# Kernel optimization log

Measured on AMD Instinct MI355X. Metric: run time of the kernel, lower is better.

The kernel has to match this reference:

```python
import jax, jax.numpy as jnp
import numpy as np
from jax import lax

P = 8  # DFFN patch_size


def _ln(x, w, b):
    # WithBias LayerNorm over channel dim of NCHW (matches to_3d -> LN(-1) -> to_4d)
    mu = x.mean(1, keepdims=True)
    var = ((x - mu) ** 2).mean(1, keepdims=True)
    return (x - mu) / jnp.sqrt(var + 1e-5) * w[None, :, None, None] + b[None, :, None, None]


def _conv1x1(x, w, b=None):
    y = jnp.einsum('bchw,oc->bohw', x, w)
    if b is not None:
        y = y + b[None, :, None, None]
    return y


def setup_inputs() -> dict:
    key = jax.random.key(0)
    ks = jax.random.split(key, 9)
    B, C, H, W = 2, 64, 96, 96
    hid = C  # ffn_expansion_factor = 1
    s = lambda k, shape, scale=0.05: jax.random.normal(k, shape, jnp.float32) * scale
    return {
        'x': s(ks[0], (B, C, H, W), 1.0),
        'ln1_w': jnp.ones((C,), jnp.float32), 'ln1_b': jnp.zeros((C,), jnp.float32),
        'ln2_w': jnp.ones((C,), jnp.float32), 'ln2_b': jnp.zeros((C,), jnp.float32),
        'q_w': s(ks[1], (C, C)), 'q_b': jnp.zeros((C,), jnp.float32),
        'k_w': s(ks[2], (C, C)), 'k_b': jnp.zeros((C,), jnp.float32),
        'v_w': s(ks[3], (C, C)), 'v_b': jnp.zeros((C,), jnp.float32),
        'fft_w': s(ks[4], (hid, P, P // 2 + 1), 1.0),
        'proj_in_w': s(ks[5], (hid, C)),
        'dw_w': s(ks[6], (hid, 1, 3, 3)),
        'proj_out_w': s(ks[7], (C, hid // 2)),
    }


def reference(x, ln1_w, ln1_b, ln2_w, ln2_b, q_w, q_b, k_w, k_b, v_w, v_b,
              fft_w, proj_in_w, dw_w, proj_out_w):
    B, C, H, W = x.shape
    # --- attention sub-block (unscaled spatial self-attn) ---
    xn = _ln(x, ln1_w, ln1_b)
    q = _conv1x1(xn, q_w, q_b).reshape(B, C, H * W)
    k = _conv1x1(xn, k_w, k_b).reshape(B, C, H * W)
    v = _conv1x1(xn, v_w, v_b).reshape(B, C, H * W)
    attn = jax.nn.softmax(jnp.einsum('bcn,bcm->bnm', q, k), axis=-1)  # [B, HW, HW]
    out = jnp.einsum('bcm,bnm->bcn', v, attn).reshape(B, C, H, W)
    x = x + out
    # --- DFFN sub-block ---
    xn = _ln(x, ln2_w, ln2_b)
    h = _conv1x1(xn, proj_in_w)  # hidden == C (expansion factor 1)
    hid = h.shape[1]
    hb, wb = H // P, W // P
    hp = h.reshape(B, hid, hb, P, wb, P).transpose(0, 2, 4, 1, 3, 5)  # [B,hb,wb,hid,P,P]
    hf = jnp.fft.rfft2(hp) * fft_w  # real learned spectral filter
    hp = jnp.fft.irfft2(hf, s=(P, P))
    h = hp.transpose(0, 3, 1, 4, 2, 5).reshape(B, hid, H, W)
    h = lax.conv_general_dilated(h, dw_w, (1, 1), ((1, 1), (1, 1)),
                                 feature_group_count=hid,
                                 dimension_numbers=('NCHW', 'OIHW', 'NCHW'))
    h1, h2 = jnp.split(h, 2, axis=1)
    h = jax.nn.gelu(h1, approximate=False) * h2  # torch F.gelu is exact erf
    return x + _conv1x1(h, proj_out_w)
```

## Files before the change

kernel.cpp:

```cpp
#include <hip/hip_runtime.h>
#include <hip/hip_bf16.h>
#include <math.h>

#define CH 64
#define NPOS 9216
#define NTOT 18432
#define NSPLIT 8
#define TILES_PER_SPLIT 18
#define LOG2E 1.4426950408889634f

typedef short bf16x8 __attribute__((ext_vector_type(8)));
typedef short bf16x4 __attribute__((ext_vector_type(4)));
typedef float f32x4 __attribute__((ext_vector_type(4)));
typedef int   i32x4 __attribute__((ext_vector_type(4)));
typedef int   i32x2 __attribute__((ext_vector_type(2)));
typedef unsigned int u32;

__device__ __forceinline__ float bf2f(short s) {
  unsigned int u = ((unsigned int)(unsigned short)s) << 16;
  return __builtin_bit_cast(float, u);
}
__device__ __forceinline__ short f2bf(float f) {
  unsigned int u = __builtin_bit_cast(unsigned int, f);
  unsigned int r = (u + 0x7fffu + ((u >> 16) & 1u)) >> 16;
  return (short)r;
}
__device__ __forceinline__ float gelu_exact(float x) {
  return 0.5f * x * (1.f + erff(x * 0.70710678118654752440f));
}


__global__ __launch_bounds__(256) void k_ln_qkv(
    const float* __restrict__ x, const float* __restrict__ ln1w, const float* __restrict__ ln1b,
    const float* __restrict__ qw, const float* __restrict__ qb,
    const float* __restrict__ kw, const float* __restrict__ kb,
    const float* __restrict__ vw, const float* __restrict__ vb,
    short* __restrict__ Qg, short* __restrict__ Kg, short* __restrict__ Vgt) {
  int mat = blockIdx.y;
  int half = blockIdx.z;
  const float* wsrc = (mat == 0) ? qw : (mat == 1) ? kw : vw;
  const float* bsrc = (mat == 0) ? qb : (mat == 1) ? kb : vb;
  int idx = blockIdx.x * 256 + threadIdx.x;
  int b = idx / NPOS, n = idx % NPOS;
  const float* xb = x + (size_t)b * CH * NPOS + n;
  float xr[64];
  float mu = 0.f;
#pragma unroll
  for (int c = 0; c < 64; ++c) { float v = xb[c * NPOS]; xr[c] = v; mu += v; }
  mu *= (1.f / 64.f);
  float var = 0.f;
#pragma unroll
  for (int c = 0; c < 64; ++c) { float d = xr[c] - mu; var += d * d; }
  float rstd = rsqrtf(var * (1.f / 64.f) + 1e-5f);
#pragma unroll
  for (int c = 0; c < 64; ++c) xr[c] = (xr[c] - mu) * rstd * ln1w[c] + ln1b[c];
  if (mat == 2) {
    for (int o2 = 0; o2 < 4; ++o2) {
#pragma unroll
      for (int j = 0; j < 8; ++j) {
        int o = half * 32 + o2 * 8 + j;
        float acc = bsrc[o];
        const float* wrow = wsrc + o * 64;
#pragma unroll
        for (int c = 0; c < 64; ++c) acc += wrow[c] * xr[c];
        Vgt[(size_t)o * NTOT + idx] = f2bf(acc);
      }
    }
  } else {
    float kscale = (mat == 1) ? LOG2E : 1.f;
    short* outp = ((mat == 0) ? Qg : Kg) + (size_t)idx * 64 + half * 32;
    for (int o2 = 0; o2 < 4; ++o2) {
      bf16x8 v8;
#pragma unroll
      for (int j = 0; j < 8; ++j) {
        int o = half * 32 + o2 * 8 + j;
        float acc = bsrc[o];
        const float* wrow = wsrc + o * 64;
#pragma unroll
        for (int c = 0; c < 64; ++c) acc += wrow[c] * xr[c];
        v8[j] = f2bf(acc * kscale);
      }
      *(bf16x8*)(outp + o2 * 8) = v8;
    }
  }
}

#define LDPK 80
#define LDP  72
__global__ __launch_bounds__(512) void k_attn(
    const short* __restrict__ Qg, const short* __restrict__ Kg, const short* __restrict__ Vgt,
    u32* __restrict__ PoT, float* __restrict__ Pl) {
  __shared__ __align__(16) short Kt[2][64 * LDPK];
  __shared__ __align__(16) short Vt[2][64 * LDP];
  int b = blockIdx.y;
  int n0 = blockIdx.x * 256;
  int ks = blockIdx.z;
  int tid = threadIdx.x;
  int w = tid >> 6, lane = tid & 63;
  int L = lane & 15, quad = lane >> 4;

  bf16x8 qa[2][2];
#pragma unroll
  for (int qt = 0; qt < 2; ++qt) {
    const short* qb_ = Qg + ((size_t)(b * NPOS + n0 + w * 32 + qt * 16 + L)) * 64;
    qa[qt][0] = *(const bf16x8*)(qb_ + quad * 8);
    qa[qt][1] = *(const bf16x8*)(qb_ + 32 + quad * 8);
  }

  f32x4 o[2][4];
#pragma unroll
  for (int qt = 0; qt < 2; ++qt)
#pragma unroll
    for (int nb = 0; nb < 4; ++nb) o[qt][nb] = (f32x4){0.f, 0.f, 0.f, 0.f};
  float rl[2] = {0.f, 0.f};

  int ck = tid & 7, rk = tid >> 3;
  int c8 = tid & 7, dr = tid >> 3;
  int vslot = (c8 >> 2) * 32 + (c8 & 1) * 16 + ((c8 >> 1) & 1) * 4;
  i32x4 kr, vr;
  {
    int kt = ks * TILES_PER_SPLIT;
    kr = ((const i32x4*)(Kg + ((size_t)(b * NPOS + kt * 64)) * 64))[tid];
    vr = *(const i32x4*)(Vgt + (size_t)b * NPOS + kt * 64 + c8 * 8 + (size_t)dr * NTOT);
    ((i32x4*)Kt[0])[rk * 10 + ck] = kr;
    short* vrow = Vt[0] + dr * LDP + vslot;
    *(i32x2*)(vrow) = (i32x2){vr[0], vr[1]};
    *(i32x2*)(vrow + 8) = (i32x2){vr[2], vr[3]};
  }

  for (int t = 0; t < TILES_PER_SPLIT; ++t) {
    int cur = t & 1;
    if (t + 1 < TILES_PER_SPLIT) {
      int kt = ks * TILES_PER_SPLIT + t + 1;
      kr = ((const i32x4*)(Kg + ((size_t)(b * NPOS + kt * 64)) * 64))[tid];
      vr = *(const i32x4*)(Vgt + (size_t)b * NPOS + kt * 64 + c8 * 8 + (size_t)dr * NTOT);
    }
    __syncthreads();

    const i32x4* kt4 = (const i32x4*)Kt[cur];
    const short* vt = Vt[cur];
    __builtin_amdgcn_s_setprio(1);
#pragma unroll
    for (int kp = 0; kp < 2; ++kp) {
      u32 pw0[4], pw1[4];
#pragma unroll
      for (int h = 0; h < 2; ++h) {
        int kti = kp * 2 + h;
        bf16x8 kf0 = __builtin_bit_cast(bf16x8, kt4[(kti * 16 + L) * 10 + quad]);
        bf16x8 kf1 = __builtin_bit_cast(bf16x8, kt4[(kti * 16 + L) * 10 + 4 + quad]);
#pragma unroll
        for (int qt = 0; qt < 2; ++qt) {
          f32x4 st = {0.f, 0.f, 0.f, 0.f};
          st = __builtin_amdgcn_mfma_f32_16x16x32_bf16(kf0, qa[qt][0], st, 0, 0, 0);
          st = __builtin_amdgcn_mfma_f32_16x16x32_bf16(kf1, qa[qt][1], st, 0, 0, 0);
          float p0 = __builtin_amdgcn_exp2f(st[0]);
          float p1 = __builtin_amdgcn_exp2f(st[1]);
          float p2 = __builtin_amdgcn_exp2f(st[2]);
          float p3 = __builtin_amdgcn_exp2f(st[3]);
          rl[qt] += (p0 + p1) + (p2 + p3);
          u32 lo = __builtin_amdgcn_perm(__builtin_bit_cast(u32, p1), __builtin_bit_cast(u32, p0), 0x07060302u);
          u32 hi = __builtin_amdgcn_perm(__builtin_bit_cast(u32, p3), __builtin_bit_cast(u32, p2), 0x07060302u);
          if (qt == 0) { pw0[h * 2] = lo; pw0[h * 2 + 1] = hi; }
          else         { pw1[h * 2] = lo; pw1[h * 2 + 1] = hi; }
        }
      }
      i32x4 pq0 = {(int)pw0[0], (int)pw0[1], (int)pw0[2], (int)pw0[3]};
      i32x4 pq1 = {(int)pw1[0], (int)pw1[1], (int)pw1[2], (int)pw1[3]};
      bf16x8 pp0 = __builtin_bit_cast(bf16x8, pq0);
      bf16x8 pp1 = __builtin_bit_cast(bf16x8, pq1);
#pragma unroll
      for (int nb = 0; nb < 4; ++nb) {
        bf16x8 va8 = *(const bf16x8*)(vt + (nb * 16 + L) * LDP + kp * 32 + quad * 8);
        o[0][nb] = __builtin_amdgcn_mfma_f32_16x16x32_bf16(va8, pp0, o[0][nb], 0, 0, 0);
        o[1][nb] = __builtin_amdgcn_mfma_f32_16x16x32_bf16(va8, pp1, o[1][nb], 0, 0, 0);
      }
    }
    __builtin_amdgcn_s_setprio(0);

    if (t + 1 < TILES_PER_SPLIT) {
      int nxt = 1 - cur;
      ((i32x4*)Kt[nxt])[rk * 10 + ck] = kr;
      short* vrow = Vt[nxt] + dr * LDP + vslot;
      *(i32x2*)(vrow) = (i32x2){vr[0], vr[1]};
      *(i32x2*)(vrow + 8) = (i32x2){vr[2], vr[3]};
    }
  }

#pragma unroll
  for (int qt = 0; qt < 2; ++qt) {
    rl[qt] += __shfl_xor(rl[qt], 16);
    rl[qt] += __shfl_xor(rl[qt], 32);
  }

#pragma unroll
  for (int qt = 0; qt < 2; ++qt) {
    int qg = b * NPOS + n0 + w * 32 + qt * 16 + L;
#pragma unroll
    for (int nb = 0; nb < 4; ++nb)
#pragma unroll
      for (int ip = 0; ip < 2; ++ip) {
        u32 pk = ((u32)(unsigned short)f2bf(o[qt][nb][2 * ip + 1]) << 16) |
                 (u32)(unsigned short)f2bf(o[qt][nb][2 * ip]);
        int d32 = nb * 8 + quad * 2 + ip;
        PoT[((size_t)(ks * 32 + d32)) * NTOT + qg] = pk;
      }
    if (quad == 0) Pl[(size_t)ks * NTOT + qg] = rl[qt];
  }
}

__global__ __launch_bounds__(256) void k_res_ln2_proj(
    const float* __restrict__ x, const u32* __restrict__ PoT, const float* __restrict__ Pl,
    const float* __restrict__ ln2w, const float* __restrict__ ln2b,
    const float* __restrict__ piw,
    float* __restrict__ X2, float* __restrict__ Hbuf) {
  __shared__ float s1a[4 * 64], s2a[4 * 64];
  __shared__ __align__(16) short xn[64 * 72];
  int t = threadIdx.x;
  int w = t >> 6;
  int p = t & 63;
  int q0 = blockIdx.x * 64;
  int q = q0 + p;
  int b = q / NPOS;
  int nn = q0 % NPOS;
  int n = q % NPOS;

  float lsum = 0.f;
#pragma unroll
  for (int s = 0; s < NSPLIT; ++s) lsum += Pl[(size_t)s * NTOT + q];
  float inv = 1.f / lsum;

  const float* xb = x + (size_t)b * CH * NPOS + n;
  float xr[16];
  float s1 = 0.f, s2 = 0.f;
#pragma unroll
  for (int j2 = 0; j2 < 8; ++j2) {
    float a0 = 0.f, a1 = 0.f;
#pragma unroll
    for (int s = 0; s < NSPLIT; ++s) {
      u32 v = PoT[((size_t)(s * 32 + w * 8 + j2)) * NTOT + q];
      a0 += __builtin_bit_cast(float, v << 16);
      a1 += __builtin_bit_cast(float, v & 0xffff0000u);
    }
    int cl = 2 * j2;
    int c = w * 16 + cl;
    float v0 = xb[(size_t)c * NPOS] + a0 * inv;
    float v1 = xb[(size_t)(c + 1) * NPOS] + a1 * inv;
    xr[cl] = v0; xr[cl + 1] = v1;
    s1 += v0 + v1;
    s2 += v0 * v0 + v1 * v1;
  }
  s1a[w * 64 + p] = s1;
  s2a[w * 64 + p] = s2;
  {
    float* xo = X2 + (size_t)b * CH * NPOS + n;
#pragma unroll
    for (int cl = 0; cl < 16; ++cl) xo[(size_t)(w * 16 + cl) * NPOS] = xr[cl];
  }
  __syncthreads();
  float mu = 0.f, m2 = 0.f;
#pragma unroll
  for (int ww = 0; ww < 4; ++ww) { mu += s1a[ww * 64 + p]; m2 += s2a[ww * 64 + p]; }
  mu *= (1.f / 64.f);
  float var = m2 * (1.f / 64.f) - mu * mu;
  float rstd = rsqrtf(var + 1e-5f);
  {
    u32* xw = (u32*)xn;
#pragma unroll
    for (int j2 = 0; j2 < 8; ++j2) {
      int cl = 2 * j2, c = w * 16 + cl;
      float y0 = (xr[cl] - mu) * rstd * ln2w[c] + ln2b[c];
      float y1 = (xr[cl + 1] - mu) * rstd * ln2w[c + 1] + ln2b[c + 1];
      u32 pk = ((u32)(unsigned short)f2bf(y1) << 16) | (u32)(unsigned short)f2bf(y0);
      xw[p * 36 + w * 8 + j2] = pk;
    }
  }
  __syncthreads();
  int lane = t & 63;
  int L = lane & 15, quad = lane >> 4;
  bf16x8 a0, a1;
  {
    const float* wr = piw + (w * 16 + L) * 64 + quad * 8;
#pragma unroll
    for (int j = 0; j < 8; ++j) { a0[j] = f2bf(wr[j]); a1[j] = f2bf(wr[32 + j]); }
  }
  float* hb = Hbuf + (size_t)b * CH * NPOS + nn;
#pragma unroll
  for (int pt = 0; pt < 4; ++pt) {
    bf16x8 b0 = *(const bf16x8*)(xn + (pt * 16 + L) * 72 + quad * 8);
    bf16x8 b1 = *(const bf16x8*)(xn + (pt * 16 + L) * 72 + 32 + quad * 8);
    f32x4 acc = {0.f, 0.f, 0.f, 0.f};
    acc = __builtin_amdgcn_mfma_f32_16x16x32_bf16(a0, b0, acc, 0, 0, 0);
    acc = __builtin_amdgcn_mfma_f32_16x16x32_bf16(a1, b1, acc, 0, 0, 0);
#pragma unroll
    for (int i = 0; i < 4; ++i)
      hb[(size_t)(w * 16 + quad * 4 + i) * NPOS + pt * 16 + L] = acc[i];
  }
}

__global__ __launch_bounds__(64) void k_fft(float* __restrict__ Hbuf, const float* __restrict__ fftw) {
  int idx = blockIdx.x * 64 + threadIdx.x;
  int wb = idx % 12;
  int t = idx / 12;
  int hb = t % 12;
  int t2 = t / 12;
  int c = t2 % 64;
  int b = t2 / 64;
  float* base = Hbuf + (size_t)(b * CH + c) * NPOS + (hb * 8) * 96 + wb * 8;
  const float r = 0.70710678118654752440f;
  const float CO[8] = {1.f, r, 0.f, -r, -1.f, -r, 0.f, r};
  const float SI[8] = {0.f, r, 1.f, r, 0.f, -r, -1.f, -r};
  float Ar[8][5], Ai[8][5];
#pragma unroll
  for (int p = 0; p < 8; ++p) {
    f32x4 ra = *(const f32x4*)(base + p * 96);
    f32x4 rb = *(const f32x4*)(base + p * 96 + 4);
    float row[8] = {ra[0], ra[1], ra[2], ra[3], rb[0], rb[1], rb[2], rb[3]};
#pragma unroll
    for (int v = 0; v < 5; ++v) {
      float sr = 0.f, si = 0.f;
#pragma unroll
      for (int q = 0; q < 8; ++q) {
        int k = (q * v) & 7;
        sr += row[q] * CO[k];
        si -= row[q] * SI[k];
      }
      Ar[p][v] = sr;
      Ai[p][v] = si;
    }
  }
  const float* wp = fftw + c * 40;
#pragma unroll
  for (int v = 0; v < 5; ++v) {
    float Br[8], Bi[8];
#pragma unroll
    for (int u = 0; u < 8; ++u) {
      float cr = 0.f, ci = 0.f;
#pragma unroll
      for (int p = 0; p < 8; ++p) {
        int k = (p * u) & 7;
        float cc = CO[k], ss = SI[k];
        cr += Ar[p][v] * cc + Ai[p][v] * ss;
        ci += Ai[p][v] * cc - Ar[p][v] * ss;
      }
      float wv = wp[u * 5 + v];
      Br[u] = cr * wv;
      Bi[u] = ci * wv;
    }
#pragma unroll
    for (int p = 0; p < 8; ++p) {
      float yr = 0.f, yi = 0.f;
#pragma unroll
      for (int u = 0; u < 8; ++u) {
        int k = (p * u) & 7;
        float cc = CO[k], ss = SI[k];
        yr += Br[u] * cc - Bi[u] * ss;
        yi += Bi[u] * cc + Br[u] * ss;
      }
      Ar[p][v] = yr * 0.125f;
      Ai[p][v] = yi * 0.125f;
    }
  }
#pragma unroll
  for (int p = 0; p < 8; ++p) {
    float outv[8];
#pragma unroll
    for (int q = 0; q < 8; ++q) {
      float acc = Ar[p][0] + ((q & 1) ? -Ar[p][4] : Ar[p][4]);
#pragma unroll
      for (int v = 1; v < 4; ++v) {
        int k = (q * v) & 7;
        acc += 2.f * (Ar[p][v] * CO[k] - Ai[p][v] * SI[k]);
      }
      outv[q] = acc * 0.125f;
    }
    f32x4 wa = {outv[0], outv[1], outv[2], outv[3]};
    f32x4 wb2 = {outv[4], outv[5], outv[6], outv[7]};
    *(f32x4*)(base + p * 96) = wa;
    *(f32x4*)(base + p * 96 + 4) = wb2;
  }
}

__global__ __launch_bounds__(256) void k_dw_gate(
    const float* __restrict__ Hbuf, const float* __restrict__ dww,
    float* __restrict__ G) {
  int cc = blockIdx.y;
  int q = blockIdx.x * 256 + threadIdx.x;
  int b = q / NPOS, n = q % NPOS;
  int y = n / 96, xx = n % 96;
  const float* h1 = Hbuf + (size_t)(b * CH + cc) * NPOS;
  const float* h2 = Hbuf + (size_t)(b * CH + cc + 32) * NPOS;
  float wd1[9], wd2[9];
#pragma unroll
  for (int ki = 0; ki < 9; ++ki) { wd1[ki] = dww[cc * 9 + ki]; wd2[ki] = dww[(cc + 32) * 9 + ki]; }
  float d1 = 0.f, d2 = 0.f;
  for (int dy = -1; dy <= 1; ++dy) {
    int yy = y + dy;
    if (yy < 0 || yy >= 96) continue;
    for (int dx = -1; dx <= 1; ++dx) {
      int xv = xx + dx;
      if (xv < 0 || xv >= 96) continue;
      int ki = (dy + 1) * 3 + (dx + 1);
      d1 += h1[yy * 96 + xv] * wd1[ki];
      d2 += h2[yy * 96 + xv] * wd2[ki];
    }
  }
  G[(size_t)cc * NTOT + q] = gelu_exact(d1) * d2;
}

__global__ __launch_bounds__(256) void k_proj_out(
    const float* __restrict__ G, const float* __restrict__ poww,
    const float* __restrict__ X2, float* __restrict__ out) {
  int og = blockIdx.y;
  int q = blockIdx.x * 256 + threadIdx.x;
  int b = q / NPOS, n = q % NPOS;
  float g[32];
#pragma unroll
  for (int cg = 0; cg < 32; ++cg) g[cg] = G[(size_t)cg * NTOT + q];
  const float* xr = X2 + (size_t)b * CH * NPOS + n;
  float* ob = out + (size_t)b * CH * NPOS + n;
#pragma unroll
  for (int j = 0; j < 8; ++j) {
    int oc = og * 8 + j;
    const float* prow = poww + oc * 32;
    float acc = xr[(size_t)oc * NPOS];
#pragma unroll
    for (int cg = 0; cg < 32; ++cg) acc += prow[cg] * g[cg];
    ob[(size_t)oc * NPOS] = acc;
  }
}

extern "C" void kernel_launch(void* const* d_in, const int* in_sizes, int n_in,
                              void* d_out, int out_size, void* d_ws, size_t ws_size,
                              hipStream_t stream) {
  const float* x    = (const float*)d_in[0];
  const float* ln1w = (const float*)d_in[1];
  const float* ln1b = (const float*)d_in[2];
  const float* ln2w = (const float*)d_in[3];
  const float* ln2b = (const float*)d_in[4];
  const float* qw   = (const float*)d_in[5];
  const float* qb   = (const float*)d_in[6];
  const float* kw   = (const float*)d_in[7];
  const float* kb   = (const float*)d_in[8];
  const float* vw   = (const float*)d_in[9];
  const float* vb   = (const float*)d_in[10];
  const float* fftw = (const float*)d_in[11];
  const float* piw  = (const float*)d_in[12];
  const float* dww  = (const float*)d_in[13];
  const float* poww = (const float*)d_in[14];

  short* Qg  = (short*)d_ws;
  short* Kg  = Qg + (size_t)NTOT * 64;
  short* Vgt = Kg + (size_t)NTOT * 64;
  u32*   PoT = (u32*)(Vgt + (size_t)NTOT * 64);
  float* Pl  = (float*)(PoT + (size_t)NSPLIT * 32 * NTOT);
  float* X2  = Pl + (size_t)NSPLIT * NTOT;
  float* Hbuf = X2 + (size_t)NTOT * 64;
  float* G   = Hbuf + (size_t)NTOT * 64;

  k_ln_qkv<<<dim3(72, 3, 2), 256, 0, stream>>>(x, ln1w, ln1b, qw, qb, kw, kb, vw, vb, Qg, Kg, Vgt);
  k_attn<<<dim3(36, 2, NSPLIT), 512, 0, stream>>>(Qg, Kg, Vgt, PoT, Pl);
  k_res_ln2_proj<<<dim3(288), 256, 0, stream>>>(x, PoT, Pl, ln2w, ln2b, piw, X2, Hbuf);
  k_fft<<<dim3(288), 64, 0, stream>>>(Hbuf, fftw);
  k_dw_gate<<<dim3(72, 32), 256, 0, stream>>>(Hbuf, dww, G);
  k_proj_out<<<dim3(72, 8), 256, 0, stream>>>(G, poww, X2, (float*)d_out);
}
```

Baseline: 195.9 us.

## Replace per-patch FFT filter with precomputed circular 8x8 spatial convolution

The rfft2, spectral multiply and irfft2 over each 8x8 patch are replaced by an equivalent circular convolution whose 8x8 spatial kernel per channel is computed from the learned spectral weights in a small new kernel. A second kernel loads each 8-row band into shared memory and does the 64-tap circular convolution per patch, with one thread per patch row. This removes the register-heavy per-thread FFT, at the cost of one extra launch and a dense 64-tap multiply-accumulate per output. The attention kernel dominates total time, so the effect on the whole is likely small.

```diff
diff --git a/kernel.cpp b/kernel.cpp
--- a/kernel.cpp
+++ b/kernel.cpp
@@ -297,87 +297,64 @@
   }
 }
 
-__global__ __launch_bounds__(64) void k_fft(float* __restrict__ Hbuf, const float* __restrict__ fftw) {
-  int idx = blockIdx.x * 64 + threadIdx.x;
-  int wb = idx % 12;
-  int t = idx / 12;
-  int hb = t % 12;
-  int t2 = t / 12;
-  int c = t2 % 64;
-  int b = t2 / 64;
-  float* base = Hbuf + (size_t)(b * CH + c) * NPOS + (hb * 8) * 96 + wb * 8;
+__global__ __launch_bounds__(64) void k_spat(
+    const float* __restrict__ fftw, float* __restrict__ ksp) {
+  int c = blockIdx.x;
+  int t = threadIdx.x;
+  int dp = t >> 3, dq = t & 7;
   const float r = 0.70710678118654752440f;
   const float CO[8] = {1.f, r, 0.f, -r, -1.f, -r, 0.f, r};
-  const float SI[8] = {0.f, r, 1.f, r, 0.f, -r, -1.f, -r};
-  float Ar[8][5], Ai[8][5];
-#pragma unroll
-  for (int p = 0; p < 8; ++p) {
-    f32x4 ra = *(const f32x4*)(base + p * 96);
-    f32x4 rb = *(const f32x4*)(base + p * 96 + 4);
-    float row[8] = {ra[0], ra[1], ra[2], ra[3], rb[0], rb[1], rb[2], rb[3]};
-#pragma unroll
-    for (int v = 0; v < 5; ++v) {
-      float sr = 0.f, si = 0.f;
-#pragma unroll
-      for (int q = 0; q < 8; ++q) {
-        int k = (q * v) & 7;
-        sr += row[q] * CO[k];
-        si -= row[q] * SI[k];
-      }
-      Ar[p][v] = sr;
-      Ai[p][v] = si;
-    }
-  }
-  const float* wp = fftw + c * 40;
-#pragma unroll
-  for (int v = 0; v < 5; ++v) {
-    float Br[8], Bi[8];
-#pragma unroll
-    for (int u = 0; u < 8; ++u) {
-      float cr = 0.f, ci = 0.f;
-#pragma unroll
-      for (int p = 0; p < 8; ++p) {
-        int k = (p * u) & 7;
-        float cc = CO[k], ss = SI[k];
-        cr += Ar[p][v] * cc + Ai[p][v] * ss;
-        ci += Ai[p][v] * cc - Ar[p][v] * ss;
-      }
-      float wv = wp[u * 5 + v];
-      Br[u] = cr * wv;
-      Bi[u] = ci * wv;
-    }
-#pragma unroll
-    for (int p = 0; p < 8; ++p) {
-      float yr = 0.f, yi = 0.f;
-#pragma unroll
-      for (int u = 0; u < 8; ++u) {
-        int k = (p * u) & 7;
-        float cc = CO[k], ss = SI[k];
-        yr += Br[u] * cc - Bi[u] * ss;
-        yi += Bi[u] * cc + Br[u] * ss;
-      }
-      Ar[p][v] = yr * 0.125f;
-      Ai[p][v] = yi * 0.125f;
-    }
-  }
-#pragma unroll
-  for (int p = 0; p < 8; ++p) {
-    float outv[8];
-#pragma unroll
-    for (int q = 0; q < 8; ++q) {
-      float acc = Ar[p][0] + ((q & 1) ? -Ar[p][4] : Ar[p][4]);
-#pragma unroll
-      for (int v = 1; v < 4; ++v) {
-        int k = (q * v) & 7;
-        acc += 2.f * (Ar[p][v] * CO[k] - Ai[p][v] * SI[k]);
-      }
-      outv[q] = acc * 0.125f;
-    }
-    f32x4 wa = {outv[0], outv[1], outv[2], outv[3]};
-    f32x4 wb2 = {outv[4], outv[5], outv[6], outv[7]};
-    *(f32x4*)(base + p * 96) = wa;
-    *(f32x4*)(base + p * 96 + 4) = wb2;
-  }
+  const float* wc = fftw + c * 40;
+  float acc = 0.f;
+#pragma unroll
+  for (int u = 0; u < 8; ++u) {
+#pragma unroll
+    for (int v = 0; v < 8; ++v) {
+      float wv = (v <= 4) ? wc[u * 5 + v] : wc[((8 - u) & 7) * 5 + (8 - v)];
+      acc += wv * CO[(u * dp + v * dq) & 7];
+    }
+  }
+  ksp[c * 64 + t] = acc * (1.f / 64.f);
+}
+
+#define LDB 100
+__global__ __launch_bounds__(96) void k_conv(
+    float* __restrict__ Hbuf, const float* __restrict__ ksp) {
+  __shared__ __align__(16) float band[8 * LDB];
+  __shared__ float kl[64];
+  int hb = blockIdx.x, c = blockIdx.y, b = blockIdx.z;
+  int t = threadIdx.x;
+  float* base = Hbuf + (size_t)(b * CH + c) * NPOS + hb * 8 * 96;
+  {
+    int sr = t / 12, sc = (t % 12) * 8;
+    f32x4 a = *(const f32x4*)(base + sr * 96 + sc);
+    f32x4 d = *(const f32x4*)(base + sr * 96 + sc + 4);
+    *(f32x4*)&band[sr * LDB + sc] = a;
+    *(f32x4*)&band[sr * LDB + sc + 4] = d;
+    if (t < 64) kl[t] = ksp[c * 64 + t];
+  }
+  __syncthreads();
+  int p = t / 12, wb = t % 12;
+  float out[8] = {0.f, 0.f, 0.f, 0.f, 0.f, 0.f, 0.f, 0.f};
+#pragma unroll
+  for (int dp = 0; dp < 8; ++dp) {
+    int rr = (p - dp) & 7;
+    f32x4 a = *(const f32x4*)&band[rr * LDB + wb * 8];
+    f32x4 d = *(const f32x4*)&band[rr * LDB + wb * 8 + 4];
+    float v[8] = {a[0], a[1], a[2], a[3], d[0], d[1], d[2], d[3]};
+    const float* krow = &kl[dp * 8];
+#pragma unroll
+    for (int dq = 0; dq < 8; ++dq) {
+      float kv = krow[dq];
+#pragma unroll
+      for (int q = 0; q < 8; ++q) out[q] += kv * v[(q - dq) & 7];
+    }
+  }
+  __syncthreads();
+  f32x4 w0 = {out[0], out[1], out[2], out[3]};
+  f32x4 w1 = {out[4], out[5], out[6], out[7]};
+  *(f32x4*)(base + p * 96 + wb * 8) = w0;
+  *(f32x4*)(base + p * 96 + wb * 8 + 4) = w1;
 }
 
 __global__ __launch_bounds__(256) void k_dw_gate(
@@ -456,11 +433,13 @@
   float* X2  = Pl + (size_t)NSPLIT * NTOT;
   float* Hbuf = X2 + (size_t)NTOT * 64;
   float* G   = Hbuf + (size_t)NTOT * 64;
-
+  float* Ksp = G + (size_t)NTOT * 32;
+
+  k_spat<<<dim3(64), 64, 0, stream>>>(fftw, Ksp);
   k_ln_qkv<<<dim3(72, 3, 2), 256, 0, stream>>>(x, ln1w, ln1b, qw, qb, kw, kb, vw, vb, Qg, Kg, Vgt);
   k_attn<<<dim3(36, 2, NSPLIT), 512, 0, stream>>>(Qg, Kg, Vgt, PoT, Pl);
   k_res_ln2_proj<<<dim3(288), 256, 0, stream>>>(x, PoT, Pl, ln2w, ln2b, piw, X2, Hbuf);
-  k_fft<<<dim3(288), 64, 0, stream>>>(Hbuf, fftw);
+  k_conv<<<dim3(12, 64, 2), 96, 0, stream>>>(Hbuf, Ksp);
   k_dw_gate<<<dim3(72, 32), 256, 0, stream>>>(Hbuf, dww, G);
   k_proj_out<<<dim3(72, 8), 256, 0, stream>>>(G, poww, X2, (float*)d_out);
 }
```

New measurement: 192.5 us. No clear change (-1.7%).
